# Kernel tuning notes

Hardware: AMD Instinct MI355X
Metric: run time of the kernel (lower is better)

The kernel has to match this reference:

```python
import jax, jax.numpy as jnp
import numpy as np

N = 131072      # octree nodes at this depth
C_IN = 256      # in_channels == out_channels
C_B = 64        # bottleneck channels = out_channels // 4
K = 27          # 3x3x3 octree kernel neighborhood
EPS = 1e-5


def _bn(x, g, b, m, v):
    # inference-style BatchNorm with given running stats
    return (x - m) * (g * jax.lax.rsqrt(v + EPS)) + b


def setup_inputs() -> dict:
    key = jax.random.key(0)
    ks = jax.random.split(key, 20)
    inp = {
        "data": jax.random.normal(ks[0], (N, C_IN), dtype=jnp.float32),
        "neigh": jax.random.randint(ks[1], (N, K), 0, N, dtype=jnp.int32),
        "depth": 6,
        # conv1x1a (Linear, no bias) + BN
        "w1": jax.random.normal(ks[2], (C_IN, C_B), dtype=jnp.float32) * 0.05,
        "bn1_g": jax.random.uniform(ks[3], (C_B,), dtype=jnp.float32) + 0.5,
        "bn1_b": jax.random.normal(ks[4], (C_B,), dtype=jnp.float32) * 0.1,
        "bn1_m": jax.random.normal(ks[5], (C_B,), dtype=jnp.float32) * 0.1,
        "bn1_v": jax.random.uniform(ks[6], (C_B,), dtype=jnp.float32) + 0.5,
        # octree conv3x3 (27-neighbor gather + GEMM, no bias) + BN
        "w3": jax.random.normal(ks[7], (K, C_B, C_B), dtype=jnp.float32) * 0.02,
        "bn2_g": jax.random.uniform(ks[8], (C_B,), dtype=jnp.float32) + 0.5,
        "bn2_b": jax.random.normal(ks[9], (C_B,), dtype=jnp.float32) * 0.1,
        "bn2_m": jax.random.normal(ks[10], (C_B,), dtype=jnp.float32) * 0.1,
        "bn2_v": jax.random.uniform(ks[11], (C_B,), dtype=jnp.float32) + 0.5,
        # conv1x1b + BN (no ReLU)
        "w2": jax.random.normal(ks[12], (C_B, C_IN), dtype=jnp.float32) * 0.05,
        "bn3_g": jax.random.uniform(ks[13], (C_IN,), dtype=jnp.float32) + 0.5,
        "bn3_b": jax.random.normal(ks[14], (C_IN,), dtype=jnp.float32) * 0.1,
        "bn3_m": jax.random.normal(ks[15], (C_IN,), dtype=jnp.float32) * 0.1,
        "bn3_v": jax.random.uniform(ks[16], (C_IN,), dtype=jnp.float32) + 0.5,
    }
    return inp


def reference(data, neigh, depth, w1, bn1_g, bn1_b, bn1_m, bn1_v,
              w3, bn2_g, bn2_b, bn2_m, bn2_v,
              w2, bn3_g, bn3_b, bn3_m, bn3_v):
    # conv1x1a + BN + ReLU
    c1 = jax.nn.relu(_bn(data @ w1, bn1_g, bn1_b, bn1_m, bn1_v))  # [N, C_B]
    # octree conv3x3: gather 27 neighbors then contract with [K, C_B, C_B]
    gathered = c1[neigh]                                          # [N, K, C_B]
    c2 = jnp.einsum('nkc,kcd->nd', gathered, w3)                  # [N, C_B]
    c2 = jax.nn.relu(_bn(c2, bn2_g, bn2_b, bn2_m, bn2_v))
    # conv1x1b + BN (no relu)
    c3 = _bn(c2 @ w2, bn3_g, bn3_b, bn3_m, bn3_v)                 # [N, C_IN]
    # residual (in_channels == out_channels -> identity shortcut) + ReLU
    return jax.nn.relu(c3 + data)
```

## Files before the change

### kernel.cpp

```cpp
#include <hip/hip_runtime.h>

#define NN 131072
#define CIN 256
#define CB 64
#define KNB 27

typedef __attribute__((ext_vector_type(8))) short short8_t;
typedef __attribute__((ext_vector_type(4))) float f32x4;

__device__ inline unsigned short f2bf(float f) {
    union { float f; unsigned u; } x; x.f = f;
    unsigned r = x.u + 0x7fffu + ((x.u >> 16) & 1u);
    return (unsigned short)(r >> 16);
}

__device__ inline f32x4 mfma16(short8_t a, short8_t b, f32x4 c) {
    return __builtin_amdgcn_mfma_f32_16x16x32_bf16(a, b, c, 0, 0, 0);
}

__global__ __launch_bounds__(256) void prep_kernel(
    const float* __restrict__ w1, const float* __restrict__ w3, const float* __restrict__ w2,
    const float* __restrict__ g1, const float* __restrict__ b1, const float* __restrict__ m1, const float* __restrict__ v1,
    const float* __restrict__ g2, const float* __restrict__ b2, const float* __restrict__ m2, const float* __restrict__ v2,
    const float* __restrict__ g3, const float* __restrict__ b3, const float* __restrict__ m3, const float* __restrict__ v3,
    unsigned short* __restrict__ w1p, unsigned short* __restrict__ w3p, unsigned short* __restrict__ w2p,
    float* __restrict__ bias1, float* __restrict__ bias2, float* __restrict__ bias3)
{
    int t = blockIdx.x * 256 + threadIdx.x;
    if (t < 16384) {
        int j = t & 7, lane = (t >> 3) & 63, tt = (t >> 9) & 3, s = t >> 11;
        int c = s * 32 + (lane >> 4) * 8 + j;
        int d = tt * 16 + (lane & 15);
        float sc = g1[d] * rsqrtf(v1[d] + 1e-5f);
        w1p[t] = f2bf(w1[c * CB + d] * sc);
    } else if (t < 16384 + 110592) {
        int u = t - 16384;
        int j = u & 7, lane = (u >> 3) & 63, tt = (u >> 9) & 3, s = (u >> 11) & 1, k = u >> 12;
        int c = s * 32 + (lane >> 4) * 8 + j;
        int d = tt * 16 + (lane & 15);
        float sc = g2[d] * rsqrtf(v2[d] + 1e-5f);
        w3p[u] = f2bf(w3[(k * CB + c) * CB + d] * sc);
    } else if (t < 143360) {
        int u = t - 126976;
        int j = u & 7, lane = (u >> 3) & 63, mt = (u >> 9) & 15, s = u >> 13;
        int c = s * 32 + (lane >> 4) * 8 + j;
        int d = mt * 16 + (lane & 15);
        float sc = g3[d] * rsqrtf(v3[d] + 1e-5f);
        w2p[u] = f2bf(w2[c * CIN + d] * sc);
    } else if (t < 143744) {
        int u = t - 143360;
        if (u < 64)       { float sc = g1[u] * rsqrtf(v1[u] + 1e-5f); bias1[u] = b1[u] - m1[u] * sc; }
        else if (u < 128) { int d = u - 64;  float sc = g2[d] * rsqrtf(v2[d] + 1e-5f); bias2[d] = b2[d] - m2[d] * sc; }
        else              { int d = u - 128; float sc = g3[d] * rsqrtf(v3[d] + 1e-5f); bias3[d] = b3[d] - m3[d] * sc; }
    }
}

__global__ __launch_bounds__(256) void k1_conv1x1a(
    const float* __restrict__ data, const unsigned short* __restrict__ w1p,
    const float* __restrict__ bias1, unsigned short* __restrict__ c1b)
{
    __shared__ short8_t w1s[2048];
    int tid = threadIdx.x;
    const short8_t* wsrc = (const short8_t*)w1p;
#pragma unroll
    for (int i = 0; i < 8; i++) w1s[tid + i * 256] = wsrc[tid + i * 256];

    int lane = tid & 63, wave = tid >> 6;
    int g = lane >> 4, r = lane & 15;
    int rowbase = blockIdx.x * 128 + wave * 32;
    f32x4 acc[2][4] = {};
    __syncthreads();

#pragma unroll
    for (int s = 0; s < 8; s++) {
        short8_t a[2];
#pragma unroll
        for (int sub = 0; sub < 2; sub++) {
            const float* ap = data + (size_t)(rowbase + sub * 16 + r) * CIN + s * 32 + g * 8;
            float4 f0 = *(const float4*)ap;
            float4 f1 = *(const float4*)(ap + 4);
            short8_t av;
            av[0] = (short)f2bf(f0.x); av[1] = (short)f2bf(f0.y);
            av[2] = (short)f2bf(f0.z); av[3] = (short)f2bf(f0.w);
            av[4] = (short)f2bf(f1.x); av[5] = (short)f2bf(f1.y);
            av[6] = (short)f2bf(f1.z); av[7] = (short)f2bf(f1.w);
            a[sub] = av;
        }
#pragma unroll
        for (int t = 0; t < 4; t++) {
            short8_t b = w1s[(s * 4 + t) * 64 + lane];
            acc[0][t] = mfma16(a[0], b, acc[0][t]);
            acc[1][t] = mfma16(a[1], b, acc[1][t]);
        }
    }

#pragma unroll
    for (int sub = 0; sub < 2; sub++)
#pragma unroll
        for (int t = 0; t < 4; t++) {
            int col = t * 16 + r;
            float bs = bias1[col];
#pragma unroll
            for (int i = 0; i < 4; i++) {
                int row = rowbase + sub * 16 + g * 4 + i;
                c1b[row * CB + col] = f2bf(fmaxf(acc[sub][t][i] + bs, 0.f));
            }
        }
}

#define K2_MFMA(aX, bX) \
    _Pragma("unroll") for (int t = 0; t < 4; t++) { \
        acc[0][t] = mfma16(aX[0], bX[t],     acc[0][t]); \
        acc[1][t] = mfma16(aX[2], bX[t],     acc[1][t]); \
        acc[0][t] = mfma16(aX[1], bX[4 + t], acc[0][t]); \
        acc[1][t] = mfma16(aX[3], bX[4 + t], acc[1][t]); \
    }

#define K23_STEP(aC, aN, ixC0, ixC1, ixN0, ixN1, k) \
    { \
        short8_t bl[8]; \
        const short8_t* bp = bbase + (size_t)(k) * 512; \
        _Pragma("unroll") for (int f = 0; f < 8; f++) bl[f] = bp[f * 64 + lane]; \
        if ((k) < 26) { \
            const short8_t* p0 = (const short8_t*)(c1b + (size_t)(ixN0) * CB); \
            const short8_t* p1 = (const short8_t*)(c1b + (size_t)(ixN1) * CB); \
            aN[0] = p0[g]; aN[1] = p0[4 + g]; aN[2] = p1[g]; aN[3] = p1[4 + g]; \
        } \
        if ((k) < 25) { ixC0 = nidx[lr0 * KNB + (k) + 2]; ixC1 = nidx[lr1 * KNB + (k) + 2]; } \
        K2_MFMA(aC, bl) \
    }

__global__ __launch_bounds__(256) void k23_fused(
    const unsigned short* __restrict__ c1b, const int* __restrict__ neigh,
    const unsigned short* __restrict__ w3p, const float* __restrict__ bias2,
    const unsigned short* __restrict__ w2p, const float* __restrict__ bias3,
    const float* __restrict__ data, float* __restrict__ out)
{
    __shared__ __align__(16) char shraw[17408];
    int* nidx = (int*)shraw;
    int tid = threadIdx.x;
    int rowbase = blockIdx.x * 128;

    const int4* nsrc = (const int4*)(neigh + (size_t)rowbase * KNB);
#pragma unroll
    for (int i = 0; i < 4; i++) {
        int p = tid + i * 256;
        if (p < 864) ((int4*)nidx)[p] = nsrc[p];
    }

    int lane = tid & 63, wave = tid >> 6;
    int g = lane >> 4, r = lane & 15;
    int lr0 = wave * 32 + r, lr1 = lr0 + 16;
    __syncthreads();

    const short8_t* bbase = (const short8_t*)w3p;
    f32x4 acc[2][4] = {};
    short8_t aA[4], aB[4];
    int ixA0, ixA1, ixB0, ixB1;

    ixA0 = nidx[lr0 * KNB + 0]; ixA1 = nidx[lr1 * KNB + 0];
    ixB0 = nidx[lr0 * KNB + 1]; ixB1 = nidx[lr1 * KNB + 1];
    {
        const short8_t* p0 = (const short8_t*)(c1b + (size_t)ixA0 * CB);
        const short8_t* p1 = (const short8_t*)(c1b + (size_t)ixA1 * CB);
        aA[0] = p0[g]; aA[1] = p0[4 + g]; aA[2] = p1[g]; aA[3] = p1[4 + g];
    }

    for (int kk = 0; kk < 13; kk++) {
        int k0 = kk * 2;
        K23_STEP(aA, aB, ixA0, ixA1, ixB0, ixB1, k0)
        K23_STEP(aB, aA, ixB0, ixB1, ixA0, ixA1, k0 + 1)
    }
    K23_STEP(aA, aB, ixA0, ixA1, ixB0, ixB1, 26)

    __syncthreads();
    unsigned short* cst = (unsigned short*)shraw + wave * 2176;
#pragma unroll
    for (int sub = 0; sub < 2; sub++)
#pragma unroll
        for (int t = 0; t < 4; t++) {
            int col = t * 16 + r;
            float bs = bias2[col];
#pragma unroll
            for (int i = 0; i < 4; i++) {
                int row = sub * 16 + g * 4 + i;
                cst[row * 68 + col] = f2bf(fmaxf(acc[sub][t][i] + bs, 0.f));
            }
        }
    __syncthreads();

    short8_t bfr[2][2];
#pragma unroll
    for (int sub = 0; sub < 2; sub++)
#pragma unroll
        for (int s = 0; s < 2; s++)
            bfr[sub][s] = *(const short8_t*)(cst + (sub * 16 + r) * 68 + s * 32 + g * 8);

    const short8_t* abase = (const short8_t*)w2p;
#pragma unroll
    for (int h = 0; h < 2; h++) {
        f32x4 acc2[2][8] = {};
#pragma unroll
        for (int mt = 0; mt < 8; mt++) {
            short8_t a0 = abase[(h * 8 + mt) * 64 + lane];
            short8_t a1 = abase[(16 + h * 8 + mt) * 64 + lane];
            acc2[0][mt] = mfma16(a0, bfr[0][0], acc2[0][mt]);
            acc2[0][mt] = mfma16(a1, bfr[0][1], acc2[0][mt]);
            acc2[1][mt] = mfma16(a0, bfr[1][0], acc2[1][mt]);
            acc2[1][mt] = mfma16(a1, bfr[1][1], acc2[1][mt]);
        }
#pragma unroll
        for (int sub = 0; sub < 2; sub++)
#pragma unroll
            for (int mt = 0; mt < 8; mt++) {
                int col0 = (h * 8 + mt) * 16 + g * 4;
                int rowg = rowbase + wave * 32 + sub * 16 + r;
                float4 bs = *(const float4*)(bias3 + col0);
                float4 dv = *(const float4*)(data + (size_t)rowg * CIN + col0);
                f32x4 v = acc2[sub][mt];
                float4 res;
                res.x = fmaxf(v[0] + bs.x + dv.x, 0.f);
                res.y = fmaxf(v[1] + bs.y + dv.y, 0.f);
                res.z = fmaxf(v[2] + bs.z + dv.z, 0.f);
                res.w = fmaxf(v[3] + bs.w + dv.w, 0.f);
                *(float4*)(out + (size_t)rowg * CIN + col0) = res;
            }
    }
}

extern "C" void kernel_launch(void* const* d_in, const int* in_sizes, int n_in,
                              void* d_out, int out_size, void* d_ws, size_t ws_size,
                              hipStream_t stream)
{
    const float* data = (const float*)d_in[0];
    const int* neigh  = (const int*)d_in[1];
    const float* w1 = (const float*)d_in[3];
    const float* g1 = (const float*)d_in[4];
    const float* b1 = (const float*)d_in[5];
    const float* m1 = (const float*)d_in[6];
    const float* v1 = (const float*)d_in[7];
    const float* w3 = (const float*)d_in[8];
    const float* g2 = (const float*)d_in[9];
    const float* b2 = (const float*)d_in[10];
    const float* m2 = (const float*)d_in[11];
    const float* v2 = (const float*)d_in[12];
    const float* w2 = (const float*)d_in[13];
    const float* g3 = (const float*)d_in[14];
    const float* b3 = (const float*)d_in[15];
    const float* m3 = (const float*)d_in[16];
    const float* v3 = (const float*)d_in[17];
    float* out = (float*)d_out;

    char* ws = (char*)d_ws;
    unsigned short* c1b = (unsigned short*)ws;
    unsigned short* w1p = (unsigned short*)(ws + 33554432);
    unsigned short* w3p = (unsigned short*)(ws + 33554432 + 32768);
    unsigned short* w2p = (unsigned short*)(ws + 33554432 + 32768 + 221184);
    float* bias1 = (float*)(ws + 33554432 + 32768 + 221184 + 32768);
    float* bias2 = bias1 + 64;
    float* bias3 = bias1 + 128;

    int n = in_sizes[0] / CIN;

    hipLaunchKernelGGL(prep_kernel, dim3(562), dim3(256), 0, stream,
                       w1, w3, w2, g1, b1, m1, v1, g2, b2, m2, v2, g3, b3, m3, v3,
                       w1p, w3p, w2p, bias1, bias2, bias3);
    hipLaunchKernelGGL(k1_conv1x1a, dim3(n / 128), dim3(256), 0, stream, data, w1p, bias1, c1b);
    hipLaunchKernelGGL(k23_fused,   dim3(n / 128), dim3(256), 0, stream,
                       c1b, neigh, w3p, bias2, w2p, bias3, data, out);
}
```

Before: 202.7 us.

## Split fused conv3x3+conv1x1b kernel and deepen gather/weight prefetch pipeline

Splits the fused k23 kernel into a conv3x3 kernel that writes a bf16 intermediate to workspace and a separate conv1x1b+residual kernel with 32-row blocks. The conv3x3 loop now triple-buffers the gathered activations and double-buffers the w3 weight fragments, prefetching one and two steps ahead to hide gather latency. This adds a 16 MB intermediate write and read plus an extra launch, in exchange for lower register pressure and better occupancy in each kernel.

```diff
diff --git a/kernel.cpp b/kernel.cpp
--- a/kernel.cpp
+++ b/kernel.cpp
@@ -108,36 +108,40 @@
         }
 }
 
-#define K2_MFMA(aX, bX) \
+#define KCLAMP(x) ((x) < 26 ? (x) : 26)
+
+#define K2_LOADB(bN, kc) { \
+    const short8_t* bp_ = bbase + (size_t)(kc) * 512; \
+    bN[0] = bp_[lane];       bN[1] = bp_[64 + lane]; \
+    bN[2] = bp_[128 + lane]; bN[3] = bp_[192 + lane]; \
+    bN[4] = bp_[256 + lane]; bN[5] = bp_[320 + lane]; \
+    bN[6] = bp_[384 + lane]; bN[7] = bp_[448 + lane]; }
+
+#define K2_GATH(aN, kc) { \
+    int i0_ = nidx[lr0 * KNB + (kc)]; \
+    int i1_ = nidx[lr1 * KNB + (kc)]; \
+    const short8_t* p0_ = (const short8_t*)(c1b + (size_t)i0_ * CB); \
+    const short8_t* p1_ = (const short8_t*)(c1b + (size_t)i1_ * CB); \
+    aN[0] = p0_[g]; aN[1] = p0_[4 + g]; aN[2] = p1_[g]; aN[3] = p1_[4 + g]; }
+
+#define K2_MF(aC, bC) { \
     _Pragma("unroll") for (int t = 0; t < 4; t++) { \
-        acc[0][t] = mfma16(aX[0], bX[t],     acc[0][t]); \
-        acc[1][t] = mfma16(aX[2], bX[t],     acc[1][t]); \
-        acc[0][t] = mfma16(aX[1], bX[4 + t], acc[0][t]); \
-        acc[1][t] = mfma16(aX[3], bX[4 + t], acc[1][t]); \
-    }
-
-#define K23_STEP(aC, aN, ixC0, ixC1, ixN0, ixN1, k) \
-    { \
-        short8_t bl[8]; \
-        const short8_t* bp = bbase + (size_t)(k) * 512; \
-        _Pragma("unroll") for (int f = 0; f < 8; f++) bl[f] = bp[f * 64 + lane]; \
-        if ((k) < 26) { \
-            const short8_t* p0 = (const short8_t*)(c1b + (size_t)(ixN0) * CB); \
-            const short8_t* p1 = (const short8_t*)(c1b + (size_t)(ixN1) * CB); \
-            aN[0] = p0[g]; aN[1] = p0[4 + g]; aN[2] = p1[g]; aN[3] = p1[4 + g]; \
-        } \
-        if ((k) < 25) { ixC0 = nidx[lr0 * KNB + (k) + 2]; ixC1 = nidx[lr1 * KNB + (k) + 2]; } \
-        K2_MFMA(aC, bl) \
-    }
-
-__global__ __launch_bounds__(256) void k23_fused(
+        acc[0][t] = mfma16(aC[0], bC[t],     acc[0][t]); \
+        acc[1][t] = mfma16(aC[2], bC[t],     acc[1][t]); \
+        acc[0][t] = mfma16(aC[1], bC[4 + t], acc[0][t]); \
+        acc[1][t] = mfma16(aC[3], bC[4 + t], acc[1][t]); } }
+
+#define K2_STEP(aC, bC, aN, bN, k) \
+    K2_LOADB(bN, KCLAMP((k) + 1)) \
+    K2_GATH(aN, KCLAMP((k) + 2)) \
+    K2_MF(aC, bC)
+
+__global__ __launch_bounds__(256) void k2_conv3x3(
     const unsigned short* __restrict__ c1b, const int* __restrict__ neigh,
     const unsigned short* __restrict__ w3p, const float* __restrict__ bias2,
-    const unsigned short* __restrict__ w2p, const float* __restrict__ bias3,
-    const float* __restrict__ data, float* __restrict__ out)
-{
-    __shared__ __align__(16) char shraw[17408];
-    int* nidx = (int*)shraw;
+    unsigned short* __restrict__ c2b)
+{
+    __shared__ int nidx[128 * KNB];
     int tid = threadIdx.x;
     int rowbase = blockIdx.x * 128;
 
@@ -155,26 +159,24 @@
 
     const short8_t* bbase = (const short8_t*)w3p;
     f32x4 acc[2][4] = {};
-    short8_t aA[4], aB[4];
-    int ixA0, ixA1, ixB0, ixB1;
-
-    ixA0 = nidx[lr0 * KNB + 0]; ixA1 = nidx[lr1 * KNB + 0];
-    ixB0 = nidx[lr0 * KNB + 1]; ixB1 = nidx[lr1 * KNB + 1];
-    {
-        const short8_t* p0 = (const short8_t*)(c1b + (size_t)ixA0 * CB);
-        const short8_t* p1 = (const short8_t*)(c1b + (size_t)ixA1 * CB);
-        aA[0] = p0[g]; aA[1] = p0[4 + g]; aA[2] = p1[g]; aA[3] = p1[4 + g];
-    }
-
-    for (int kk = 0; kk < 13; kk++) {
-        int k0 = kk * 2;
-        K23_STEP(aA, aB, ixA0, ixA1, ixB0, ixB1, k0)
-        K23_STEP(aB, aA, ixB0, ixB1, ixA0, ixA1, k0 + 1)
-    }
-    K23_STEP(aA, aB, ixA0, ixA1, ixB0, ixB1, 26)
-
-    __syncthreads();
-    unsigned short* cst = (unsigned short*)shraw + wave * 2176;
+    short8_t aA[4], aB[4], aC[4], bX[8], bY[8];
+
+    K2_LOADB(bX, 0)
+    K2_GATH(aA, 0)
+    K2_GATH(aB, 1)
+
+    for (int kb = 0; kb < 24; kb += 6) {
+        K2_STEP(aA, bX, aC, bY, kb + 0)
+        K2_STEP(aB, bY, aA, bX, kb + 1)
+        K2_STEP(aC, bX, aB, bY, kb + 2)
+        K2_STEP(aA, bY, aC, bX, kb + 3)
+        K2_STEP(aB, bX, aA, bY, kb + 4)
+        K2_STEP(aC, bY, aB, bX, kb + 5)
+    }
+    K2_STEP(aA, bX, aC, bY, 24)
+    K2_STEP(aB, bY, aA, bX, 25)
+    K2_STEP(aC, bX, aB, bY, 26)
+
 #pragma unroll
     for (int sub = 0; sub < 2; sub++)
 #pragma unroll
@@ -183,49 +185,57 @@
             float bs = bias2[col];
 #pragma unroll
             for (int i = 0; i < 4; i++) {
-                int row = sub * 16 + g * 4 + i;
-                cst[row * 68 + col] = f2bf(fmaxf(acc[sub][t][i] + bs, 0.f));
+                int row = rowbase + wave * 32 + sub * 16 + g * 4 + i;
+                c2b[row * CB + col] = f2bf(fmaxf(acc[sub][t][i] + bs, 0.f));
             }
         }
-    __syncthreads();
-
+}
+
+__global__ __launch_bounds__(256) void k3_conv1x1b(
+    const unsigned short* __restrict__ c2b, const unsigned short* __restrict__ w2p,
+    const float* __restrict__ bias3, const float* __restrict__ data,
+    float* __restrict__ out)
+{
+    int tid = threadIdx.x;
+    int lane = tid & 63, wave = tid >> 6;
+    int g = lane >> 4, r = lane & 15;
+    int rowbase = blockIdx.x * 32;
+
+    const short8_t* abase = (const short8_t*)w2p;
     short8_t bfr[2][2];
 #pragma unroll
     for (int sub = 0; sub < 2; sub++)
 #pragma unroll
         for (int s = 0; s < 2; s++)
-            bfr[sub][s] = *(const short8_t*)(cst + (sub * 16 + r) * 68 + s * 32 + g * 8);
-
-    const short8_t* abase = (const short8_t*)w2p;
-#pragma unroll
-    for (int h = 0; h < 2; h++) {
-        f32x4 acc2[2][8] = {};
-#pragma unroll
-        for (int mt = 0; mt < 8; mt++) {
-            short8_t a0 = abase[(h * 8 + mt) * 64 + lane];
-            short8_t a1 = abase[(16 + h * 8 + mt) * 64 + lane];
-            acc2[0][mt] = mfma16(a0, bfr[0][0], acc2[0][mt]);
-            acc2[0][mt] = mfma16(a1, bfr[0][1], acc2[0][mt]);
-            acc2[1][mt] = mfma16(a0, bfr[1][0], acc2[1][mt]);
-            acc2[1][mt] = mfma16(a1, bfr[1][1], acc2[1][mt]);
-        }
-#pragma unroll
-        for (int sub = 0; sub < 2; sub++)
-#pragma unroll
-            for (int mt = 0; mt < 8; mt++) {
-                int col0 = (h * 8 + mt) * 16 + g * 4;
-                int rowg = rowbase + wave * 32 + sub * 16 + r;
-                float4 bs = *(const float4*)(bias3 + col0);
-                float4 dv = *(const float4*)(data + (size_t)rowg * CIN + col0);
-                f32x4 v = acc2[sub][mt];
-                float4 res;
-                res.x = fmaxf(v[0] + bs.x + dv.x, 0.f);
-                res.y = fmaxf(v[1] + bs.y + dv.y, 0.f);
-                res.z = fmaxf(v[2] + bs.z + dv.z, 0.f);
-                res.w = fmaxf(v[3] + bs.w + dv.w, 0.f);
-                *(float4*)(out + (size_t)rowg * CIN + col0) = res;
-            }
-    }
+            bfr[sub][s] = *(const short8_t*)(c2b + (size_t)(rowbase + sub * 16 + r) * CB + s * 32 + g * 8);
+
+    f32x4 acc2[2][4] = {};
+#pragma unroll
+    for (int mt = 0; mt < 4; mt++) {
+        short8_t a0 = abase[(wave * 4 + mt) * 64 + lane];
+        short8_t a1 = abase[(16 + wave * 4 + mt) * 64 + lane];
+        acc2[0][mt] = mfma16(a0, bfr[0][0], acc2[0][mt]);
+        acc2[0][mt] = mfma16(a1, bfr[0][1], acc2[0][mt]);
+        acc2[1][mt] = mfma16(a0, bfr[1][0], acc2[1][mt]);
+        acc2[1][mt] = mfma16(a1, bfr[1][1], acc2[1][mt]);
+    }
+
+#pragma unroll
+    for (int sub = 0; sub < 2; sub++)
+#pragma unroll
+        for (int mt = 0; mt < 4; mt++) {
+            int col0 = (wave * 4 + mt) * 16 + g * 4;
+            int rowg = rowbase + sub * 16 + r;
+            float4 bs = *(const float4*)(bias3 + col0);
+            float4 dv = *(const float4*)(data + (size_t)rowg * CIN + col0);
+            f32x4 v = acc2[sub][mt];
+            float4 res;
+            res.x = fmaxf(v[0] + bs.x + dv.x, 0.f);
+            res.y = fmaxf(v[1] + bs.y + dv.y, 0.f);
+            res.z = fmaxf(v[2] + bs.z + dv.z, 0.f);
+            res.w = fmaxf(v[3] + bs.w + dv.w, 0.f);
+            *(float4*)(out + (size_t)rowg * CIN + col0) = res;
+        }
 }
 
 extern "C" void kernel_launch(void* const* d_in, const int* in_sizes, int n_in,
@@ -253,6 +263,7 @@
 
     char* ws = (char*)d_ws;
     unsigned short* c1b = (unsigned short*)ws;
+    unsigned short* c2b = (unsigned short*)(ws + 16777216);
     unsigned short* w1p = (unsigned short*)(ws + 33554432);
     unsigned short* w3p = (unsigned short*)(ws + 33554432 + 32768);
     unsigned short* w2p = (unsigned short*)(ws + 33554432 + 32768 + 221184);
@@ -266,6 +277,6 @@
                        w1, w3, w2, g1, b1, m1, v1, g2, b2, m2, v2, g3, b3, m3, v3,
                        w1p, w3p, w2p, bias1, bias2, bias3);
     hipLaunchKernelGGL(k1_conv1x1a, dim3(n / 128), dim3(256), 0, stream, data, w1p, bias1, c1b);
-    hipLaunchKernelGGL(k23_fused,   dim3(n / 128), dim3(256), 0, stream,
-                       c1b, neigh, w3p, bias2, w2p, bias3, data, out);
-}
+    hipLaunchKernelGGL(k2_conv3x3,  dim3(n / 128), dim3(256), 0, stream, c1b, neigh, w3p, bias2, c2b);
+    hipLaunchKernelGGL(k3_conv1x1b, dim3(n / 32),  dim3(256), 0, stream, c2b, w2p, bias3, data, out);
+}
```

Measured after the change: 190.0 us. 1.07x faster.
